# Optimization experiments

Hardware: AMD Instinct MI355X
Metric: run time of the kernel (lower is better)

Reference implementation:

```python
import jax, jax.numpy as jnp
import numpy as np

MODES = 16   # hard-coded in FNO(..., modes=16, width=32)
WIDTH = 32


def setup_inputs() -> dict:
    key = jax.random.key(0)
    ks = jax.random.split(key, 13)
    B, S, IN, E, OUT, L = 4, 256, 1024, 2048, 1024, 4
    s = 0.02
    return {
        "x": jax.random.normal(ks[0], (B, S, IN), jnp.float32),
        "W_en": jax.random.normal(ks[1], (IN, E), jnp.float32) * s,
        "b_en": jnp.zeros((E,), jnp.float32),
        "fc0_w": jax.random.normal(ks[2], (L, 1, WIDTH), jnp.float32) * s,
        "fc0_b": jnp.zeros((L, WIDTH), jnp.float32),
        "spec_wr": jax.random.normal(ks[3], (L, WIDTH, WIDTH, MODES), jnp.float32) / WIDTH,
        "spec_wi": jax.random.normal(ks[4], (L, WIDTH, WIDTH, MODES), jnp.float32) / WIDTH,
        "pw_w": jax.random.normal(ks[5], (L, WIDTH, WIDTH), jnp.float32) * s,
        "pw_b": jnp.zeros((L, WIDTH), jnp.float32),
        "fc1_w": jax.random.normal(ks[6], (L, WIDTH, 1), jnp.float32) * s,
        "fc1_b": jnp.zeros((L, 1), jnp.float32),
        "W_de": jax.random.normal(ks[7], (E, OUT), jnp.float32) * s,
        "b_de": jnp.zeros((OUT,), jnp.float32),
    }


def _fno_block(u, fc0_w, fc0_b, wr, wi, pw_w, pw_b, fc1_w, fc1_b):
    # u: (T, E, 1) -- 1 channel over spatial axis E
    v = u @ fc0_w + fc0_b                       # (T, E, WIDTH) channel lift
    Vf = jnp.fft.rfft(v, axis=1)                # (T, E//2+1, WIDTH) complex
    Wc = wr + 1j * wi                           # (WIDTH, WIDTH, MODES)
    out_m = jnp.einsum("tmc,cdm->tmd", Vf[:, :MODES, :], Wc)
    Of = jnp.zeros_like(Vf).at[:, :MODES, :].set(out_m)
    v1 = jnp.fft.irfft(Of, n=v.shape[1], axis=1)  # spectral conv branch
    v2 = v @ pw_w + pw_b                          # pointwise 1x1 conv branch
    v = jax.nn.gelu(v1 + v2)
    return v @ fc1_w + fc1_b                      # (T, E, 1) channel project


def reference(x, W_en, b_en, fc0_w, fc0_b, spec_wr, spec_wi, pw_w, pw_b, fc1_w, fc1_b, W_de, b_de):
    h = x @ W_en + b_en                          # (B, S, E)
    B, S, E = h.shape
    u = h.reshape(B * S, E, 1)                   # embed axis = FNO spatial axis, 1 channel
    L = fc0_w.shape[0]
    for i in range(L):                           # small fixed layer count
        u = _fno_block(u, fc0_w[i], fc0_b[i], spec_wr[i], spec_wi[i],
                       pw_w[i], pw_b[i], fc1_w[i], fc1_b[i])
    h = u.reshape(B, S, E)
    return h @ W_de + b_de                       # (B, S, OUT)
```

## Files before the change

### kernel.cpp

```cpp
#include <hip/hip_runtime.h>
#include <math.h>

#ifndef M_PI
#define M_PI 3.14159265358979323846
#endif

#define T_ROWS 1024
#define EDIM   2048
#define IN_DIM 1024
#define OUT_DIM 1024
#define NMODES 16
#define NLAYERS 4

typedef __attribute__((ext_vector_type(8))) short bf16x8;
typedef __attribute__((ext_vector_type(4))) float f32x4;

__device__ __forceinline__ unsigned short f2bf(float f) {
  union { float f; unsigned u; } v; v.f = f;
  unsigned r = v.u + 0x7FFFu + ((v.u >> 16) & 1u);
  return (unsigned short)(r >> 16);
}
__device__ __forceinline__ float bf2f(unsigned short h) {
  union { unsigned u; float f; } v; v.u = ((unsigned)h) << 16;
  return v.f;
}
__device__ __forceinline__ void f2bf_split(float v, unsigned short& h, unsigned short& l) {
  h = f2bf(v);
  l = f2bf(v - bf2f(h));
}

__device__ __forceinline__ void transpose_tile(const float* __restrict__ B,
                                               unsigned short* __restrict__ BT,
                                               int K, int N, int k0, int n0, int tid,
                                               float (*tile)[33])
{
  {
    int r = tid >> 3, c4 = (tid & 7) * 4;
    float4 v = *(const float4*)&B[(size_t)(k0 + r) * N + n0 + c4];
    tile[r][c4 + 0] = v.x; tile[r][c4 + 1] = v.y;
    tile[r][c4 + 2] = v.z; tile[r][c4 + 3] = v.w;
  }
  __syncthreads();
  {
    int n = tid >> 3, kq = (tid & 7) * 4;
    ushort4 o;
    o.x = f2bf(tile[kq + 0][n]); o.y = f2bf(tile[kq + 1][n]);
    o.z = f2bf(tile[kq + 2][n]); o.w = f2bf(tile[kq + 3][n]);
    *(ushort4*)&BT[(size_t)(n0 + n) * K + k0 + kq] = o;
  }
}

__global__ __launch_bounds__(256)
void setup_all(float* __restrict__ ctab, float* __restrict__ stab,
               unsigned short* __restrict__ basFh, unsigned short* __restrict__ basFl,
               const float* __restrict__ fc0w, const float* __restrict__ fc0b,
               const float* __restrict__ wr, const float* __restrict__ wi,
               const float* __restrict__ pww, const float* __restrict__ pwb,
               float* __restrict__ Wmr, float* __restrict__ Wmi,
               float* __restrict__ b0r, float* __restrict__ pw1,
               float* __restrict__ pb1,
               const float* __restrict__ W_en, unsigned short* __restrict__ WenT,
               const float* __restrict__ W_de, unsigned short* __restrict__ WdeT,
               const float* __restrict__ x, unsigned short* __restrict__ x_bf)
{
  __shared__ float tile[32][33];
  const int b = blockIdx.x, tid = threadIdx.x;
  if (b < 8) {
    int i = b * 256 + tid;
    double ang = (2.0 * M_PI / (double)EDIM) * (double)i;
    ctab[i] = (float)cos(ang);
    stab[i] = (float)sin(ang);
  } else if (b < 264) {
    int idx = (b - 8) * 256 + tid;
    int mt = idx >> 9;
    int l  = (idx >> 3) & 63;
    int i  = idx & 7;
    int xx = mt * 16 + (l & 15);
    int j  = (l >> 4) * 8 + i;
    float v;
    if (j < 31) {
      int m = (j < NMODES) ? j : (j - 15);
      int ia = (m * xx) & (EDIM - 1);
      double ang = (2.0 * M_PI / (double)EDIM) * (double)ia;
      v = (j < NMODES) ? (float)cos(ang) : (float)sin(ang);
    } else {
      v = 1.0f;
    }
    unsigned short h, lo; f2bf_split(v, h, lo);
    basFh[idx] = h; basFl[idx] = lo;
  } else if (b == 264) {
    if (tid >= NLAYERS * 32) return;
    int l = tid >> 5, d = tid & 31;
    for (int m = 0; m < NMODES; ++m) {
      float sr = 0.f, si = 0.f;
      for (int c = 0; c < 32; ++c) {
        float w0 = fc0w[l * 32 + c];
        size_t base = ((size_t)(l * 32 + c) * 32 + d) * NMODES + m;
        sr += w0 * wr[base];
        si += w0 * wi[base];
      }
      Wmr[(l * NMODES + m) * 32 + d] = sr;
      Wmi[(l * NMODES + m) * 32 + d] = si;
    }
    float sb = 0.f, sp = 0.f, sq = 0.f;
    for (int c = 0; c < 32; ++c) {
      float b0 = fc0b[l * 32 + c];
      float w0 = fc0w[l * 32 + c];
      sb += b0 * wr[((size_t)(l * 32 + c) * 32 + d) * NMODES + 0];
      float pw = pww[(size_t)(l * 32 + c) * 32 + d];
      sp += w0 * pw;
      sq += b0 * pw;
    }
    b0r[l * 32 + d] = (float)EDIM * sb;
    pw1[l * 32 + d] = sp;
    pb1[l * 32 + d] = sq + pwb[l * 32 + d];
  } else if (b < 2313) {
    int tb = b - 265;
    int n0 = (tb & 63) * 32, k0 = (tb >> 6) * 32;
    transpose_tile(W_en, WenT, IN_DIM, EDIM, k0, n0, tid, tile);
  } else if (b < 4361) {
    int tb = b - 2313;
    int n0 = (tb & 31) * 32, k0 = (tb >> 5) * 32;
    transpose_tile(W_de, WdeT, EDIM, OUT_DIM, k0, n0, tid, tile);
  } else {
    size_t i0 = ((size_t)(b - 4361) * 256 + tid) * 8;
    float4 a0 = *(const float4*)&x[i0];
    float4 a1 = *(const float4*)&x[i0 + 4];
    ushort4 o0, o1;
    o0.x = f2bf(a0.x); o0.y = f2bf(a0.y); o0.z = f2bf(a0.z); o0.w = f2bf(a0.w);
    o1.x = f2bf(a1.x); o1.y = f2bf(a1.y); o1.z = f2bf(a1.z); o1.w = f2bf(a1.w);
    *(ushort4*)&x_bf[i0]     = o0;
    *(ushort4*)&x_bf[i0 + 4] = o1;
  }
}

#define BKK 64
__global__ __launch_bounds__(256)
void gemm_mfma(const unsigned short* __restrict__ A, const unsigned short* __restrict__ BT,
               const float* __restrict__ bias, float* __restrict__ C,
               int M, int N, int K)
{
  __shared__ __align__(16) unsigned short Asb[64 * BKK];
  __shared__ __align__(16) unsigned short Bsb[64 * BKK];
  const int tid = threadIdx.x;
  const int bm = blockIdx.y * 64, bn = blockIdx.x * 64;
  const int lane = tid & 63, wave = tid >> 6;
  const int wr = wave >> 1, wc = wave & 1;

  const int srow = tid >> 2;
  const int skq  = tid & 3;

  f32x4 acc[2][2] = {};

  const unsigned short* aRow = A + (size_t)(bm + srow) * K + skq * 16;
  const unsigned short* bRow = BT + (size_t)(bn + srow) * K + skq * 16;

  for (int k0 = 0; k0 < K; k0 += BKK) {
    #pragma unroll
    for (int h = 0; h < 2; ++h) {
      int kb = skq * 2 + h;
      int slot = kb ^ ((srow >> 1) & 7);
      *(bf16x8*)&Asb[srow * BKK + slot * 8] = *(const bf16x8*)(aRow + k0 + h * 8);
      *(bf16x8*)&Bsb[srow * BKK + slot * 8] = *(const bf16x8*)(bRow + k0 + h * 8);
    }
    __syncthreads();
    #pragma unroll
    for (int s = 0; s < 2; ++s) {
      int kb = s * 4 + (lane >> 4);
      bf16x8 a[2], b[2];
      #pragma unroll
      for (int i = 0; i < 2; ++i) {
        int ar = wr * 32 + i * 16 + (lane & 15);
        a[i] = *(const bf16x8*)&Asb[ar * BKK + (kb ^ ((ar >> 1) & 7)) * 8];
        int br = wc * 32 + i * 16 + (lane & 15);
        b[i] = *(const bf16x8*)&Bsb[br * BKK + (kb ^ ((br >> 1) & 7)) * 8];
      }
      #pragma unroll
      for (int i = 0; i < 2; ++i)
        #pragma unroll
        for (int j = 0; j < 2; ++j)
          acc[i][j] = __builtin_amdgcn_mfma_f32_16x16x32_bf16(a[i], b[j], acc[i][j], 0, 0, 0);
    }
    __syncthreads();
  }

  #pragma unroll
  for (int j = 0; j < 2; ++j) {
    int col = bn + wc * 32 + j * 16 + (lane & 15);
    float bz = bias[col];
    #pragma unroll
    for (int i = 0; i < 2; ++i)
      #pragma unroll
      for (int r = 0; r < 4; ++r) {
        int row = bm + wr * 32 + i * 16 + (lane >> 4) * 4 + r;
        C[(size_t)row * N + col] = acc[i][j][r] + bz;
      }
  }
}

__global__ __launch_bounds__(256)
void dft0(const float* __restrict__ u,
          const float* __restrict__ ctab, const float* __restrict__ stab,
          float* __restrict__ UrOut)
{
  const int t = blockIdx.x, tid = threadIdx.x;
  __shared__ float red[4][32];

  float pr[NMODES], pi[NMODES];
  #pragma unroll
  for (int m = 0; m < NMODES; ++m) { pr[m] = 0.f; pi[m] = 0.f; }
  #pragma unroll
  for (int it = 0; it < 8; ++it) {
    const int x = tid + it * 256;
    const float val = u[(size_t)t * EDIM + x];
    const float cx = ctab[x], sx = stab[x];
    float c = 1.f, s = 0.f;
    #pragma unroll
    for (int m = 0; m < NMODES; ++m) {
      pr[m] += val * c;
      pi[m] -= val * s;
      float cn = c * cx - s * sx;
      s = s * cx + c * sx;
      c = cn;
    }
  }
  #pragma unroll
  for (int m = 0; m < NMODES; ++m) {
    #pragma unroll
    for (int off = 32; off > 0; off >>= 1) {
      pr[m] += __shfl_down(pr[m], off, 64);
      pi[m] += __shfl_down(pi[m], off, 64);
    }
  }
  int lane = tid & 63, wid = tid >> 6;
  if (lane == 0) {
    #pragma unroll
    for (int m = 0; m < NMODES; ++m) { red[wid][m] = pr[m]; red[wid][NMODES + m] = pi[m]; }
  }
  __syncthreads();
  if (tid < 32) UrOut[t * 32 + tid] = red[0][tid] + red[1][tid] + red[2][tid] + red[3][tid];
}

template<int LAST>
__global__ __launch_bounds__(256, 4)
void recon_mfma(float* __restrict__ u,
                unsigned short* __restrict__ u_bf,
                const float* __restrict__ UrIn,
                float* __restrict__ UrOut,
                const unsigned short* __restrict__ basFh,
                const unsigned short* __restrict__ basFl,
                const float* __restrict__ ctab, const float* __restrict__ stab,
                const float* __restrict__ Wmr, const float* __restrict__ Wmi,
                const float* __restrict__ b0r, const float* __restrict__ pb1,
                const float* __restrict__ pw1,
                const float* __restrict__ f1w, const float* __restrict__ f1b)
{
  const int t = blockIdx.x;
  const int tid = threadIdx.x, lane = tid & 63, w = tid >> 6;
  const int g = lane >> 4, m15 = lane & 15;

  __shared__ float urow[EDIM];
  __shared__ float Ush[32];
  __shared__ float red[4][32];
  __shared__ __align__(16) unsigned short cfh[2][64][8];
  __shared__ __align__(16) unsigned short cfl[2][64][8];

  {
    const float4* us = (const float4*)(u + (size_t)t * EDIM);
    ((float4*)urow)[tid]       = us[tid];
    ((float4*)urow)[tid + 256] = us[tid + 256];
  }
  if (tid < 32) Ush[tid] = UrIn[t * 32 + tid];
  __syncthreads();

  if (tid < 128) {
    const float invN = 1.0f / (float)EDIM;
    int n = tid >> 6, ll = tid & 63;
    int d = n * 16 + (ll & 15);
    #pragma unroll
    for (int i = 0; i < 8; ++i) {
      int j = (ll >> 4) * 8 + i;
      float v;
      if (j < NMODES) {
        int m = j;
        float ofr = Ush[m] * Wmr[m * 32 + d] - Ush[NMODES + m] * Wmi[m * 32 + d];
        v = (m == 0) ? (ofr + b0r[d]) * invN : 2.0f * ofr * invN;
      } else if (j < 31) {
        int m = j - 15;
        float ofi = Ush[m] * Wmi[m * 32 + d] + Ush[NMODES + m] * Wmr[m * 32 + d];
        v = -2.0f * ofi * invN;
      } else {
        v = pb1[d];
      }
      f2bf_split(v, cfh[n][ll][i], cfl[n][ll][i]);
    }
  }
  __syncthreads();

  bf16x8 ch[2], cl[2];
  #pragma unroll
  for (int n = 0; n < 2; ++n) {
    ch[n] = *(const bf16x8*)&cfh[n][lane][0];
    cl[n] = *(const bf16x8*)&cfl[n][lane][0];
  }
  float4 pwv[2], fv[2];
  #pragma unroll
  for (int n = 0; n < 2; ++n) {
    pwv[n] = *(const float4*)&pw1[n * 16 + g * 4];
    fv[n]  = *(const float4*)&f1w[n * 16 + g * 4];
  }
  const float fb = f1b[0];

  #pragma unroll 4
  for (int c = 0; c < 32; ++c) {
    const int mt = w * 32 + c;
    bf16x8 bh = *(const bf16x8*)&basFh[((size_t)mt * 64 + lane) * 8];
    bf16x8 bl = *(const bf16x8*)&basFl[((size_t)mt * 64 + lane) * 8];
    f32x4 acc[2];
    #pragma unroll
    for (int n = 0; n < 2; ++n) {
      f32x4 a = {};
      a = __builtin_amdgcn_mfma_f32_16x16x32_bf16(cl[n], bh, a, 0, 0, 0);
      a = __builtin_amdgcn_mfma_f32_16x16x32_bf16(ch[n], bl, a, 0, 0, 0);
      a = __builtin_amdgcn_mfma_f32_16x16x32_bf16(ch[n], bh, a, 0, 0, 0);
      acc[n] = a;
    }
    const int x = mt * 16 + m15;
    const float uval = urow[x];
    float o = 0.f;
    #pragma unroll
    for (int n = 0; n < 2; ++n) {
      #pragma unroll
      for (int r = 0; r < 4; ++r) {
        float s = fmaf(uval, ((const float*)&pwv[n])[r], acc[n][r]);
        float s2 = s * s;
        float arg = s * fmaf(0.1029433f, s2, 2.3022082f);
        float e2 = __builtin_amdgcn_exp2f(arg);
        float r1 = __builtin_amdgcn_rcpf(e2 + 1.0f);
        float sf = s * ((const float*)&fv[n])[r];
        o += sf;
        o = fmaf(-sf, r1, o);
      }
    }
    o += __shfl_xor(o, 16, 64);
    o += __shfl_xor(o, 32, 64);
    if (lane < 16) urow[x] = o + fb;
  }
  __syncthreads();

  if (LAST) {
    float4 a0 = ((const float4*)urow)[tid];
    float4 a1 = ((const float4*)urow)[tid + 256];
    ushort4 o0, o1;
    o0.x = f2bf(a0.x); o0.y = f2bf(a0.y); o0.z = f2bf(a0.z); o0.w = f2bf(a0.w);
    o1.x = f2bf(a1.x); o1.y = f2bf(a1.y); o1.z = f2bf(a1.z); o1.w = f2bf(a1.w);
    *(ushort4*)&u_bf[(size_t)t * EDIM + tid * 4]        = o0;
    *(ushort4*)&u_bf[(size_t)t * EDIM + 1024 + tid * 4] = o1;
  } else {
    float pr[NMODES], pi[NMODES];
    #pragma unroll
    for (int m = 0; m < NMODES; ++m) { pr[m] = 0.f; pi[m] = 0.f; }
    #pragma unroll
    for (int it = 0; it < 8; ++it) {
      const int x = tid + it * 256;
      const float val = urow[x];
      const float cx = ctab[x], sx = stab[x];
      float c = 1.f, s = 0.f;
      #pragma unroll
      for (int m = 0; m < NMODES; ++m) {
        pr[m] += val * c;
        pi[m] -= val * s;
        float cn = c * cx - s * sx;
        s = s * cx + c * sx;
        c = cn;
      }
    }
    #pragma unroll
    for (int m = 0; m < NMODES; ++m) {
      #pragma unroll
      for (int off = 32; off > 0; off >>= 1) {
        pr[m] += __shfl_down(pr[m], off, 64);
        pi[m] += __shfl_down(pi[m], off, 64);
      }
    }
    if (lane == 0) {
      #pragma unroll
      for (int m = 0; m < NMODES; ++m) { red[w][m] = pr[m]; red[w][NMODES + m] = pi[m]; }
    }
    __syncthreads();
    if (tid < 32) UrOut[t * 32 + tid] = red[0][tid] + red[1][tid] + red[2][tid] + red[3][tid];
    float4* ud = (float4*)(u + (size_t)t * EDIM);
    ud[tid]       = ((const float4*)urow)[tid];
    ud[tid + 256] = ((const float4*)urow)[tid + 256];
  }
}

extern "C" void kernel_launch(void* const* d_in, const int* in_sizes, int n_in,
                              void* d_out, int out_size, void* d_ws, size_t ws_size,
                              hipStream_t stream)
{
  const float* x    = (const float*)d_in[0];
  const float* W_en = (const float*)d_in[1];
  const float* b_en = (const float*)d_in[2];
  const float* fc0w = (const float*)d_in[3];
  const float* fc0b = (const float*)d_in[4];
  const float* swr  = (const float*)d_in[5];
  const float* swi  = (const float*)d_in[6];
  const float* pww  = (const float*)d_in[7];
  const float* pwb  = (const float*)d_in[8];
  const float* f1w  = (const float*)d_in[9];
  const float* f1b  = (const float*)d_in[10];
  const float* W_de = (const float*)d_in[11];
  const float* b_de = (const float*)d_in[12];
  float* out = (float*)d_out;
  float* ws  = (float*)d_ws;

  float* u    = ws;
  float* ctab = u + (size_t)T_ROWS * EDIM;
  float* stab = ctab + EDIM;
  float* Wmr  = stab + EDIM;
  float* Wmi  = Wmr + NLAYERS * NMODES * 32;
  float* b0r  = Wmi + NLAYERS * NMODES * 32;
  float* pw1  = b0r + NLAYERS * 32;
  float* pb1  = pw1 + NLAYERS * 32;
  float* UrA  = pb1 + NLAYERS * 32;
  float* UrB  = UrA + T_ROWS * 32;
  unsigned short* basFh = (unsigned short*)(UrB + T_ROWS * 32);
  unsigned short* basFl = basFh + 128 * 64 * 8;
  unsigned short* x_bf  = basFl + 128 * 64 * 8;
  unsigned short* u_bf  = x_bf + (size_t)T_ROWS * IN_DIM;
  unsigned short* WenT  = u_bf + (size_t)T_ROWS * EDIM;
  unsigned short* WdeT  = WenT + (size_t)EDIM * IN_DIM;

  setup_all<<<4873, 256, 0, stream>>>(ctab, stab, basFh, basFl, fc0w, fc0b,
                                      swr, swi, pww, pwb, Wmr, Wmi, b0r, pw1, pb1,
                                      W_en, WenT, W_de, WdeT, x, x_bf);

  { dim3 g(EDIM / 64, T_ROWS / 64);
    gemm_mfma<<<g, 256, 0, stream>>>(x_bf, WenT, b_en, u, T_ROWS, EDIM, IN_DIM); }

  dft0<<<T_ROWS, 256, 0, stream>>>(u, ctab, stab, UrA);

  for (int l = 0; l < NLAYERS; ++l) {
    const float* UrIn  = (l & 1) ? UrB : UrA;
    float*       UrOut = (l & 1) ? UrA : UrB;
    if (l < NLAYERS - 1)
      recon_mfma<0><<<T_ROWS, 256, 0, stream>>>(u, u_bf, UrIn, UrOut,
          basFh, basFl, ctab, stab,
          Wmr + l * NMODES * 32, Wmi + l * NMODES * 32, b0r + l * 32, pb1 + l * 32,
          pw1 + l * 32, f1w + l * 32, f1b + l);
    else
      recon_mfma<1><<<T_ROWS, 256, 0, stream>>>(u, u_bf, UrIn, UrOut,
          basFh, basFl, ctab, stab,
          Wmr + l * NMODES * 32, Wmi + l * NMODES * 32, b0r + l * 32, pb1 + l * 32,
          pw1 + l * 32, f1w + l * 32, f1b + l);
  }

  { dim3 g(OUT_DIM / 64, T_ROWS / 64);
    gemm_mfma<<<g, 256, 0, stream>>>(u_bf, WdeT, b_de, out, T_ROWS, OUT_DIM, EDIM); }
}
```

Before: 249.7 us.

## Split each row's DFT and reconstruction across four blocks with partial mode sums

The dft0 and recon_mfma kernels now launch four blocks per row, each handling a 512-element quarter of the spatial axis. Each block writes partial Fourier mode sums to a quadrupled workspace, and the next layer adds the four partials when loading modes. The aim is more parallelism and smaller shared memory per block, so more blocks fit on the GPU at once. In exchange, every block redoes the mode-coefficient setup, reads more partial data and pays more launch and sync overhead per block.

Measured after the change: 305.4 us. 1.22x slower.

```diff
diff --git a/kernel.cpp b/kernel.cpp
--- a/kernel.cpp
+++ b/kernel.cpp
@@ -203,15 +203,15 @@
           const float* __restrict__ ctab, const float* __restrict__ stab,
           float* __restrict__ UrOut)
 {
-  const int t = blockIdx.x, tid = threadIdx.x;
+  const int t = blockIdx.x >> 2, cq = blockIdx.x & 3, tid = threadIdx.x;
   __shared__ float red[4][32];
 
   float pr[NMODES], pi[NMODES];
   #pragma unroll
   for (int m = 0; m < NMODES; ++m) { pr[m] = 0.f; pi[m] = 0.f; }
   #pragma unroll
-  for (int it = 0; it < 8; ++it) {
-    const int x = tid + it * 256;
+  for (int it = 0; it < 2; ++it) {
+    const int x = cq * 512 + tid + it * 256;
     const float val = u[(size_t)t * EDIM + x];
     const float cx = ctab[x], sx = stab[x];
     float c = 1.f, s = 0.f;
@@ -238,7 +238,9 @@
     for (int m = 0; m < NMODES; ++m) { red[wid][m] = pr[m]; red[wid][NMODES + m] = pi[m]; }
   }
   __syncthreads();
-  if (tid < 32) UrOut[t * 32 + tid] = red[0][tid] + red[1][tid] + red[2][tid] + red[3][tid];
+  if (tid < 32)
+    UrOut[((size_t)cq * T_ROWS + t) * 32 + tid] =
+        red[0][tid] + red[1][tid] + red[2][tid] + red[3][tid];
 }
 
 template<int LAST>
@@ -255,22 +257,22 @@
                 const float* __restrict__ pw1,
                 const float* __restrict__ f1w, const float* __restrict__ f1b)
 {
-  const int t = blockIdx.x;
+  const int t = blockIdx.x >> 2, cq = blockIdx.x & 3;
   const int tid = threadIdx.x, lane = tid & 63, w = tid >> 6;
   const int g = lane >> 4, m15 = lane & 15;
 
-  __shared__ float urow[EDIM];
+  __shared__ float urow[512];
   __shared__ float Ush[32];
   __shared__ float red[4][32];
   __shared__ __align__(16) unsigned short cfh[2][64][8];
   __shared__ __align__(16) unsigned short cfl[2][64][8];
 
-  {
-    const float4* us = (const float4*)(u + (size_t)t * EDIM);
-    ((float4*)urow)[tid]       = us[tid];
-    ((float4*)urow)[tid + 256] = us[tid + 256];
-  }
-  if (tid < 32) Ush[tid] = UrIn[t * 32 + tid];
+  ((float2*)urow)[tid] = ((const float2*)(u + (size_t)t * EDIM + cq * 512))[tid];
+  if (tid < 32) {
+    const size_t o = (size_t)t * 32 + tid;
+    Ush[tid] = UrIn[o] + UrIn[(size_t)T_ROWS * 32 + o]
+             + UrIn[2 * (size_t)T_ROWS * 32 + o] + UrIn[3 * (size_t)T_ROWS * 32 + o];
+  }
   __syncthreads();
 
   if (tid < 128) {
@@ -311,59 +313,60 @@
   }
   const float fb = f1b[0];
 
-  #pragma unroll 4
-  for (int c = 0; c < 32; ++c) {
-    const int mt = w * 32 + c;
-    bf16x8 bh = *(const bf16x8*)&basFh[((size_t)mt * 64 + lane) * 8];
-    bf16x8 bl = *(const bf16x8*)&basFl[((size_t)mt * 64 + lane) * 8];
-    f32x4 acc[2];
-    #pragma unroll
-    for (int n = 0; n < 2; ++n) {
-      f32x4 a = {};
-      a = __builtin_amdgcn_mfma_f32_16x16x32_bf16(cl[n], bh, a, 0, 0, 0);
-      a = __builtin_amdgcn_mfma_f32_16x16x32_bf16(ch[n], bl, a, 0, 0, 0);
-      a = __builtin_amdgcn_mfma_f32_16x16x32_bf16(ch[n], bh, a, 0, 0, 0);
-      acc[n] = a;
-    }
-    const int x = mt * 16 + m15;
-    const float uval = urow[x];
-    float o = 0.f;
-    #pragma unroll
-    for (int n = 0; n < 2; ++n) {
-      #pragma unroll
-      for (int r = 0; r < 4; ++r) {
-        float s = fmaf(uval, ((const float*)&pwv[n])[r], acc[n][r]);
-        float s2 = s * s;
-        float arg = s * fmaf(0.1029433f, s2, 2.3022082f);
-        float e2 = __builtin_amdgcn_exp2f(arg);
-        float r1 = __builtin_amdgcn_rcpf(e2 + 1.0f);
-        float sf = s * ((const float*)&fv[n])[r];
-        o += sf;
-        o = fmaf(-sf, r1, o);
-      }
-    }
-    o += __shfl_xor(o, 16, 64);
-    o += __shfl_xor(o, 32, 64);
-    if (lane < 16) urow[x] = o + fb;
+  #pragma unroll 2
+  for (int c2 = 0; c2 < 2; ++c2) {
+    #pragma unroll
+    for (int q = 0; q < 4; ++q) {
+      const int mtl = w * 8 + c2 * 4 + q;
+      const int mt = cq * 32 + mtl;
+      bf16x8 bh = *(const bf16x8*)&basFh[((size_t)mt * 64 + lane) * 8];
+      bf16x8 bl = *(const bf16x8*)&basFl[((size_t)mt * 64 + lane) * 8];
+      f32x4 acc[2];
+      #pragma unroll
+      for (int n = 0; n < 2; ++n) {
+        f32x4 a = {};
+        a = __builtin_amdgcn_mfma_f32_16x16x32_bf16(cl[n], bh, a, 0, 0, 0);
+        a = __builtin_amdgcn_mfma_f32_16x16x32_bf16(ch[n], bl, a, 0, 0, 0);
+        a = __builtin_amdgcn_mfma_f32_16x16x32_bf16(ch[n], bh, a, 0, 0, 0);
+        acc[n] = a;
+      }
+      const int xl = mtl * 16 + m15;
+      const float uval = urow[xl];
+      float o = 0.f;
+      #pragma unroll
+      for (int n = 0; n < 2; ++n) {
+        #pragma unroll
+        for (int r = 0; r < 4; ++r) {
+          float s = fmaf(uval, ((const float*)&pwv[n])[r], acc[n][r]);
+          float s2 = s * s;
+          float arg = s * fmaf(0.1029433f, s2, 2.3022082f);
+          float e2 = __builtin_amdgcn_exp2f(arg);
+          float r1 = __builtin_amdgcn_rcpf(e2 + 1.0f);
+          float sf = s * ((const float*)&fv[n])[r];
+          o += sf;
+          o = fmaf(-sf, r1, o);
+        }
+      }
+      o += __shfl_xor(o, 16, 64);
+      o += __shfl_xor(o, 32, 64);
+      if (lane < 16) urow[xl] = o + fb;
+    }
   }
   __syncthreads();
 
   if (LAST) {
-    float4 a0 = ((const float4*)urow)[tid];
-    float4 a1 = ((const float4*)urow)[tid + 256];
-    ushort4 o0, o1;
-    o0.x = f2bf(a0.x); o0.y = f2bf(a0.y); o0.z = f2bf(a0.z); o0.w = f2bf(a0.w);
-    o1.x = f2bf(a1.x); o1.y = f2bf(a1.y); o1.z = f2bf(a1.z); o1.w = f2bf(a1.w);
-    *(ushort4*)&u_bf[(size_t)t * EDIM + tid * 4]        = o0;
-    *(ushort4*)&u_bf[(size_t)t * EDIM + 1024 + tid * 4] = o1;
+    float2 a = ((const float2*)urow)[tid];
+    ushort2 ob; ob.x = f2bf(a.x); ob.y = f2bf(a.y);
+    *(ushort2*)&u_bf[(size_t)t * EDIM + cq * 512 + tid * 2] = ob;
   } else {
     float pr[NMODES], pi[NMODES];
     #pragma unroll
     for (int m = 0; m < NMODES; ++m) { pr[m] = 0.f; pi[m] = 0.f; }
     #pragma unroll
-    for (int it = 0; it < 8; ++it) {
-      const int x = tid + it * 256;
-      const float val = urow[x];
+    for (int it = 0; it < 2; ++it) {
+      const int xl = tid + it * 256;
+      const int x = cq * 512 + xl;
+      const float val = urow[xl];
       const float cx = ctab[x], sx = stab[x];
       float c = 1.f, s = 0.f;
       #pragma unroll
@@ -388,10 +391,10 @@
       for (int m = 0; m < NMODES; ++m) { red[w][m] = pr[m]; red[w][NMODES + m] = pi[m]; }
     }
     __syncthreads();
-    if (tid < 32) UrOut[t * 32 + tid] = red[0][tid] + red[1][tid] + red[2][tid] + red[3][tid];
-    float4* ud = (float4*)(u + (size_t)t * EDIM);
-    ud[tid]       = ((const float4*)urow)[tid];
-    ud[tid + 256] = ((const float4*)urow)[tid + 256];
+    if (tid < 32)
+      UrOut[((size_t)cq * T_ROWS + t) * 32 + tid] =
+          red[0][tid] + red[1][tid] + red[2][tid] + red[3][tid];
+    ((float2*)(u + (size_t)t * EDIM + cq * 512))[tid] = ((const float2*)urow)[tid];
   }
 }
 
@@ -424,8 +427,8 @@
   float* pw1  = b0r + NLAYERS * 32;
   float* pb1  = pw1 + NLAYERS * 32;
   float* UrA  = pb1 + NLAYERS * 32;
-  float* UrB  = UrA + T_ROWS * 32;
-  unsigned short* basFh = (unsigned short*)(UrB + T_ROWS * 32);
+  float* UrB  = UrA + 4 * (size_t)T_ROWS * 32;
+  unsigned short* basFh = (unsigned short*)(UrB + 4 * (size_t)T_ROWS * 32);
   unsigned short* basFl = basFh + 128 * 64 * 8;
   unsigned short* x_bf  = basFl + 128 * 64 * 8;
   unsigned short* u_bf  = x_bf + (size_t)T_ROWS * IN_DIM;
@@ -439,18 +442,18 @@
   { dim3 g(EDIM / 64, T_ROWS / 64);
     gemm_mfma<<<g, 256, 0, stream>>>(x_bf, WenT, b_en, u, T_ROWS, EDIM, IN_DIM); }
 
-  dft0<<<T_ROWS, 256, 0, stream>>>(u, ctab, stab, UrA);
+  dft0<<<4 * T_ROWS, 256, 0, stream>>>(u, ctab, stab, UrA);
 
   for (int l = 0; l < NLAYERS; ++l) {
     const float* UrIn  = (l & 1) ? UrB : UrA;
     float*       UrOut = (l & 1) ? UrA : UrB;
     if (l < NLAYERS - 1)
-      recon_mfma<0><<<T_ROWS, 256, 0, stream>>>(u, u_bf, UrIn, UrOut,
+      recon_mfma<0><<<4 * T_ROWS, 256, 0, stream>>>(u, u_bf, UrIn, UrOut,
           basFh, basFl, ctab, stab,
           Wmr + l * NMODES * 32, Wmi + l * NMODES * 32, b0r + l * 32, pb1 + l * 32,
           pw1 + l * 32, f1w + l * 32, f1b + l);
     else
-      recon_mfma<1><<<T_ROWS, 256, 0, stream>>>(u, u_bf, UrIn, UrOut,
+      recon_mfma<1><<<4 * T_ROWS, 256, 0, stream>>>(u, u_bf, UrIn, UrOut,
           basFh, basFl, ctab, stab,
           Wmr + l * NMODES * 32, Wmi + l * NMODES * 32, b0r + l * 32, pb1 + l * 32,
           pw1 + l * 32, f1w + l * 32, f1b + l);
```
